# Performance work log

Hardware: AMD Instinct MI355X
Metric: run time of the kernel (lower is better)

## Reference

```python
import jax, jax.numpy as jnp
import numpy as np

B, C, RES, N_ANGLES = 32, 16, 128, 64


def setup_inputs() -> dict:
    key = jax.random.key(0)
    k1, k2, k3 = jax.random.split(key, 3)
    x = jax.random.normal(k1, (B, C, RES, RES), dtype=jnp.float32)
    # torch-radon setup: angles = np.linspace(0, 2*pi, 64)
    angles = jnp.linspace(0.0, 2.0 * np.pi, N_ANGLES).astype(jnp.float32)
    # Conv2d(16, 1, 1) params (kaiming-ish scale)
    conv_w = jax.random.normal(k2, (1, C, 1, 1), dtype=jnp.float32) * (1.0 / np.sqrt(C))
    conv_b = jax.random.normal(k3, (1,), dtype=jnp.float32) * 0.01
    return {"x": x, "angles": angles, "conv_w": conv_w, "conv_b": conv_b}


def _radon(x, angles):
    # x: (B, C, H, W) -> sinogram (B, C, n_angles, det_count)
    H = x.shape[-2]
    W = x.shape[-1]
    center = (H - 1) / 2.0
    # detector positions s and ray-integration positions t, in pixel units, centered
    coords = jnp.arange(H, dtype=jnp.float32) - center  # (RES,)

    def proj_one(carry, theta):
        c, s = jnp.cos(theta), jnp.sin(theta)
        # rotated sampling grid: (D, T) = (detector, along-ray)
        xs = coords[:, None] * c - coords[None, :] * s + center
        ys = coords[:, None] * s + coords[None, :] * c + center
        x0 = jnp.floor(xs)
        y0 = jnp.floor(ys)
        wx = xs - x0  # bilinear weights
        wy = ys - y0
        x0i = x0.astype(jnp.int32)
        y0i = y0.astype(jnp.int32)

        def g(yi, xi):
            # zero-padded gather: (B, C, D, T)
            valid = ((yi >= 0) & (yi < H) & (xi >= 0) & (xi < W)).astype(x.dtype)
            v = x[:, :, jnp.clip(yi, 0, H - 1), jnp.clip(xi, 0, W - 1)]
            return v * valid

        val = (g(y0i, x0i) * ((1.0 - wy) * (1.0 - wx))
               + g(y0i, x0i + 1) * ((1.0 - wy) * wx)
               + g(y0i + 1, x0i) * (wy * (1.0 - wx))
               + g(y0i + 1, x0i + 1) * (wy * wx))
        # line integral: sum along the ray (T axis) -> (B, C, D)
        return carry, val.sum(axis=-1)

    _, sino = jax.lax.scan(proj_one, 0, angles)  # (A, B, C, D)
    return jnp.transpose(sino, (1, 2, 0, 3))      # (B, C, A, D)


def reference(x, angles, conv_w, conv_b):
    sino = _radon(x, angles)  # (B, C, A, D)
    # 1x1 conv: contract channel dim
    out = jnp.einsum('bcad,oc->boad', sino, conv_w[:, :, 0, 0])
    return out + conv_b[None, :, None, None]
```

## Files before the change

### kernel.cpp

```cpp
#include <hip/hip_runtime.h>


#define B_    32
#define C_    16
#define RES   128
#define NA    64
#define SLDS  133
#define ROWS  132
#define NELEM (ROWS * SLDS)
#define NPAD  18432
#define NPAIR 16

typedef _Float16 half2v __attribute__((ext_vector_type(2)));

__global__ __launch_bounds__(256) void chan_reduce(const float* __restrict__ x,
                                                   const float* __restrict__ w,
                                                   float* __restrict__ y) {
    int t  = blockIdx.x * 256 + threadIdx.x;
    int b  = t >> 12;
    int r4 = t & 4095;
    const float4* xb = (const float4*)(x + (size_t)b * C_ * RES * RES);
    float wr[C_];
#pragma unroll
    for (int c = 0; c < C_; ++c) wr[c] = w[c];
    float4 acc = make_float4(0.f, 0.f, 0.f, 0.f);
#pragma unroll
    for (int c = 0; c < C_; ++c) {
        float4 v = xb[c * (RES * RES / 4) + r4];
        acc.x = fmaf(wr[c], v.x, acc.x);
        acc.y = fmaf(wr[c], v.y, acc.y);
        acc.z = fmaf(wr[c], v.z, acc.z);
        acc.w = fmaf(wr[c], v.w, acc.w);
    }
    ((float4*)y)[(size_t)b * (RES * RES / 4) + r4] = acc;
}

__global__ __launch_bounds__(256) void pack_pairs(const float* __restrict__ y,
                                                  uint2* __restrict__ pk) {
    int flat = blockIdx.x * 256 + threadIdx.x;
    int p    = flat / NPAD;
    int rem  = flat - p * NPAD;
    uint2 val = make_uint2(0u, 0u);
    if (rem < NELEM) {
        int r = rem / SLDS;
        int c = rem - r * SLDS;
        if (r >= 2 && r <= 129 && c >= 1 && c <= 129) {
            int q = r - 2;
            int m = c - 2;
            const float* y0 = y + (size_t)(2 * p) * (RES * RES) + q * RES;
            const float* y1 = y0 + RES * RES;
            float a0 = (m >= 0)  ? y0[m]     : 0.f;
            float a1 = (m < 127) ? y0[m + 1] : 0.f;
            float b0 = (m >= 0)  ? y1[m]     : 0.f;
            float b1 = (m < 127) ? y1[m + 1] : 0.f;
            val.x = __builtin_bit_cast(unsigned int, __builtin_amdgcn_cvt_pkrtz(a0, a1));
            val.y = __builtin_bit_cast(unsigned int, __builtin_amdgcn_cvt_pkrtz(b0, b1));
        }
    }
    pk[flat] = val;
}

__global__ __launch_bounds__(512) void radon_k(const uint2* __restrict__ pk,
                                               const float* __restrict__ angles,
                                               const float* __restrict__ bias,
                                               float* __restrict__ out) {
    __shared__ uint2 lds[NPAD];
    const int bid = blockIdx.x;
    const int p   = bid >> 4;
    const int grp = bid & 15;
    const int t   = threadIdx.x;

    {
        const uint4* src = (const uint4*)(pk + (size_t)p * NPAD);
        uint4*       dst = (uint4*)lds;
#pragma unroll
        for (int k = 0; k < 18; ++k) dst[k * 512 + t] = src[k * 512 + t];
    }
    __syncthreads();

    const int a = (t >> 7) * 16 + grp;
    const int i = t & 127;
    float th = angles[a];
    float s, c;
    __sincosf(th, &s, &c);

    const float ci = (float)i - 63.5f;
    const float Xb = fmaf(ci, c, fmaf(63.5f, s, 65.5f));
    const float Yb = fmaf(ci, s, fmaf(-63.5f, c, 65.5f));
    const float ns = -s;

    float acc00 = 0.f, acc01 = 0.f, acc10 = 0.f, acc11 = 0.f;
#pragma unroll 8
    for (int j = 0; j < RES; ++j) {
        float jf = (float)j;
        float X  = fmaf(jf, ns, Xb);
        float Y  = fmaf(jf, c,  Yb);
        float fx = floorf(X), fy = floorf(Y);
        float wx = X - fx,    wy = Y - fy;
        float gx = fminf(fmaxf(fx, 0.f), 130.f);
        float gy = fminf(fmaxf(fy, 0.f), 130.f);
        int addr = (int)fmaf(gy, (float)SLDS, gx);
        uint2 q0 = lds[addr];
        uint2 q1 = lds[addr + SLDS];
        float u  = 1.f - wx;
        float A0 = 1.f - wy;
        half2v wa = __builtin_bit_cast(half2v, __builtin_amdgcn_cvt_pkrtz(A0 * u, A0 * wx));
        half2v wb = __builtin_bit_cast(half2v, __builtin_amdgcn_cvt_pkrtz(wy * u, wy * wx));
        acc00 = __builtin_amdgcn_fdot2(__builtin_bit_cast(half2v, q0.x), wa, acc00, false);
        acc10 = __builtin_amdgcn_fdot2(__builtin_bit_cast(half2v, q0.y), wa, acc10, false);
        acc01 = __builtin_amdgcn_fdot2(__builtin_bit_cast(half2v, q1.x), wb, acc01, false);
        acc11 = __builtin_amdgcn_fdot2(__builtin_bit_cast(half2v, q1.y), wb, acc11, false);
    }

    float bv = bias[0];
    out[(2 * p)     * (NA * RES) + a * RES + i] = (acc00 + acc01) + bv;
    out[(2 * p + 1) * (NA * RES) + a * RES + i] = (acc10 + acc11) + bv;
}

extern "C" void kernel_launch(void* const* d_in, const int* in_sizes, int n_in,
                              void* d_out, int out_size, void* d_ws, size_t ws_size,
                              hipStream_t stream) {
    const float* x      = (const float*)d_in[0];
    const float* angles = (const float*)d_in[1];
    const float* w      = (const float*)d_in[2];
    const float* bias   = (const float*)d_in[3];
    float* out = (float*)d_out;

    float* y  = (float*)d_ws;
    uint2* pk = (uint2*)((char*)d_ws + (size_t)4 * 1024 * 1024);

    chan_reduce<<<dim3(512), dim3(256), 0, stream>>>(x, w, y);
    pack_pairs<<<dim3(NPAIR * NPAD / 256), dim3(256), 0, stream>>>(y, pk);
    radon_k<<<dim3(NPAIR * 16), dim3(512), 0, stream>>>(pk, angles, bias, out);
}
```

Before: 98.05 us.

## Pack per-pixel batch pairs in LDS, split rays in halves with atomics, use packed fp16 FMA

The LDS image layout changes from storing horizontal neighbour pairs for two batches (uint2) to one packed fp16 pair of the two batches per pixel (uint32), which halves LDS size to 72 KB. That lets more blocks fit per CU, and launch_bounds now requests 4. Each ray is split into two halves handled by separate blocks, doubling the grid. Partial sums are combined with atomicAdd into an output zeroed by a new memset. Accumulation now uses packed fp16 FMA over 8 steps before promoting to fp32, which trades accuracy for fewer instructions and adds four LDS loads per sample instead of two.

```diff
diff --git a/kernel.cpp b/kernel.cpp
--- a/kernel.cpp
+++ b/kernel.cpp
@@ -8,7 +8,7 @@
 #define SLDS  133
 #define ROWS  132
 #define NELEM (ROWS * SLDS)
-#define NPAD  18432
+#define NPADE 18432
 #define NPAIR 16
 
 typedef _Float16 half2v __attribute__((ext_vector_type(2)));
@@ -36,45 +36,41 @@
 }
 
 __global__ __launch_bounds__(256) void pack_pairs(const float* __restrict__ y,
-                                                  uint2* __restrict__ pk) {
+                                                  unsigned int* __restrict__ pk) {
     int flat = blockIdx.x * 256 + threadIdx.x;
-    int p    = flat / NPAD;
-    int rem  = flat - p * NPAD;
-    uint2 val = make_uint2(0u, 0u);
+    int p    = flat / NPADE;
+    int rem  = flat - p * NPADE;
+    unsigned int val = 0u;
     if (rem < NELEM) {
         int r = rem / SLDS;
         int c = rem - r * SLDS;
-        if (r >= 2 && r <= 129 && c >= 1 && c <= 129) {
-            int q = r - 2;
-            int m = c - 2;
+        if (r >= 2 && r <= 129 && c >= 2 && c <= 129) {
+            int q = r - 2, m = c - 2;
             const float* y0 = y + (size_t)(2 * p) * (RES * RES) + q * RES;
             const float* y1 = y0 + RES * RES;
-            float a0 = (m >= 0)  ? y0[m]     : 0.f;
-            float a1 = (m < 127) ? y0[m + 1] : 0.f;
-            float b0 = (m >= 0)  ? y1[m]     : 0.f;
-            float b1 = (m < 127) ? y1[m + 1] : 0.f;
-            val.x = __builtin_bit_cast(unsigned int, __builtin_amdgcn_cvt_pkrtz(a0, a1));
-            val.y = __builtin_bit_cast(unsigned int, __builtin_amdgcn_cvt_pkrtz(b0, b1));
+            val = __builtin_bit_cast(unsigned int,
+                      __builtin_amdgcn_cvt_pkrtz(y0[m], y1[m]));
         }
     }
     pk[flat] = val;
 }
 
-__global__ __launch_bounds__(512) void radon_k(const uint2* __restrict__ pk,
-                                               const float* __restrict__ angles,
-                                               const float* __restrict__ bias,
-                                               float* __restrict__ out) {
-    __shared__ uint2 lds[NPAD];
+__global__ __launch_bounds__(512, 4) void radon_k(const unsigned int* __restrict__ pk,
+                                                  const float* __restrict__ angles,
+                                                  const float* __restrict__ bias,
+                                                  float* __restrict__ out) {
+    __shared__ unsigned int lds[NPADE];
     const int bid = blockIdx.x;
-    const int p   = bid >> 4;
-    const int grp = bid & 15;
+    const int h   = bid & 1;
+    const int grp = (bid >> 1) & 15;
+    const int p   = bid >> 5;
     const int t   = threadIdx.x;
 
     {
-        const uint4* src = (const uint4*)(pk + (size_t)p * NPAD);
+        const uint4* src = (const uint4*)(pk + (size_t)p * NPADE);
         uint4*       dst = (uint4*)lds;
 #pragma unroll
-        for (int k = 0; k < 18; ++k) dst[k * 512 + t] = src[k * 512 + t];
+        for (int k = 0; k < 9; ++k) dst[k * 512 + t] = src[k * 512 + t];
     }
     __syncthreads();
 
@@ -85,36 +81,46 @@
     __sincosf(th, &s, &c);
 
     const float ci = (float)i - 63.5f;
-    const float Xb = fmaf(ci, c, fmaf(63.5f, s, 65.5f));
-    const float Yb = fmaf(ci, s, fmaf(-63.5f, c, 65.5f));
+    const float j0 = (float)(h * 64);
+    const float Xb = fmaf(ci, c, fmaf(63.5f - j0, s, 65.5f));
+    const float Yb = fmaf(ci, s, fmaf(j0 - 63.5f, c, 65.5f));
     const float ns = -s;
 
-    float acc00 = 0.f, acc01 = 0.f, acc10 = 0.f, acc11 = 0.f;
-#pragma unroll 8
-    for (int j = 0; j < RES; ++j) {
-        float jf = (float)j;
-        float X  = fmaf(jf, ns, Xb);
-        float Y  = fmaf(jf, c,  Yb);
-        float fx = floorf(X), fy = floorf(Y);
-        float wx = X - fx,    wy = Y - fy;
-        float gx = fminf(fmaxf(fx, 0.f), 130.f);
-        float gy = fminf(fmaxf(fy, 0.f), 130.f);
-        int addr = (int)fmaf(gy, (float)SLDS, gx);
-        uint2 q0 = lds[addr];
-        uint2 q1 = lds[addr + SLDS];
-        float u  = 1.f - wx;
-        float A0 = 1.f - wy;
-        half2v wa = __builtin_bit_cast(half2v, __builtin_amdgcn_cvt_pkrtz(A0 * u, A0 * wx));
-        half2v wb = __builtin_bit_cast(half2v, __builtin_amdgcn_cvt_pkrtz(wy * u, wy * wx));
-        acc00 = __builtin_amdgcn_fdot2(__builtin_bit_cast(half2v, q0.x), wa, acc00, false);
-        acc10 = __builtin_amdgcn_fdot2(__builtin_bit_cast(half2v, q0.y), wa, acc10, false);
-        acc01 = __builtin_amdgcn_fdot2(__builtin_bit_cast(half2v, q1.x), wb, acc01, false);
-        acc11 = __builtin_amdgcn_fdot2(__builtin_bit_cast(half2v, q1.y), wb, acc11, false);
+    float accf0 = 0.f, accf1 = 0.f;
+#pragma unroll
+    for (int o = 0; o < 8; ++o) {
+        half2v accA = (half2v)0, accB = (half2v)0;
+#pragma unroll
+        for (int u8 = 0; u8 < 8; ++u8) {
+            float jf = (float)(o * 8 + u8);
+            float X  = fmaf(jf, ns, Xb);
+            float Y  = fmaf(jf, c,  Yb);
+            float fx = floorf(X), fy = floorf(Y);
+            float wx = X - fx,    wy = Y - fy;
+            float gx = fminf(fmaxf(fx, 0.f), 130.f);
+            float gy = fminf(fmaxf(fy, 0.f), 130.f);
+            int addr = (int)fmaf(gy, (float)SLDS, gx);
+            unsigned int q00 = lds[addr],        q01 = lds[addr + 1];
+            unsigned int q10 = lds[addr + SLDS], q11 = lds[addr + SLDS + 1];
+            float un = 1.f - wx;
+            float A0 = 1.f - wy;
+            half2v w00 = __builtin_bit_cast(half2v, __builtin_amdgcn_cvt_pkrtz(A0 * un, A0 * un));
+            half2v w01 = __builtin_bit_cast(half2v, __builtin_amdgcn_cvt_pkrtz(A0 * wx, A0 * wx));
+            half2v w10 = __builtin_bit_cast(half2v, __builtin_amdgcn_cvt_pkrtz(wy * un, wy * un));
+            half2v w11 = __builtin_bit_cast(half2v, __builtin_amdgcn_cvt_pkrtz(wy * wx, wy * wx));
+            accA = __builtin_elementwise_fma(__builtin_bit_cast(half2v, q00), w00, accA);
+            accA = __builtin_elementwise_fma(__builtin_bit_cast(half2v, q01), w01, accA);
+            accB = __builtin_elementwise_fma(__builtin_bit_cast(half2v, q10), w10, accB);
+            accB = __builtin_elementwise_fma(__builtin_bit_cast(half2v, q11), w11, accB);
+        }
+        half2v accp = accA + accB;
+        accf0 += (float)accp.x;
+        accf1 += (float)accp.y;
     }
 
-    float bv = bias[0];
-    out[(2 * p)     * (NA * RES) + a * RES + i] = (acc00 + acc01) + bv;
-    out[(2 * p + 1) * (NA * RES) + a * RES + i] = (acc10 + acc11) + bv;
+    float bv = (h == 0) ? bias[0] : 0.f;
+    atomicAdd(&out[(2 * p)     * (NA * RES) + a * RES + i], accf0 + bv);
+    atomicAdd(&out[(2 * p + 1) * (NA * RES) + a * RES + i], accf1 + bv);
 }
 
 extern "C" void kernel_launch(void* const* d_in, const int* in_sizes, int n_in,
@@ -126,10 +132,11 @@
     const float* bias   = (const float*)d_in[3];
     float* out = (float*)d_out;
 
-    float* y  = (float*)d_ws;
-    uint2* pk = (uint2*)((char*)d_ws + (size_t)4 * 1024 * 1024);
+    float*        y  = (float*)d_ws;
+    unsigned int* pk = (unsigned int*)((char*)d_ws + (size_t)4 * 1024 * 1024);
 
+    hipMemsetAsync(out, 0, (size_t)out_size * sizeof(float), stream);
     chan_reduce<<<dim3(512), dim3(256), 0, stream>>>(x, w, y);
-    pack_pairs<<<dim3(NPAIR * NPAD / 256), dim3(256), 0, stream>>>(y, pk);
-    radon_k<<<dim3(NPAIR * 16), dim3(512), 0, stream>>>(pk, angles, bias, out);
+    pack_pairs<<<dim3(NPAIR * NPADE / 256), dim3(256), 0, stream>>>(y, pk);
+    radon_k<<<dim3(NPAIR * 16 * 2), dim3(512), 0, stream>>>(pk, angles, bias, out);
 }
```

New measurement: 300.4 us. +206.4%, slower.
